# Performance work log

Hardware: AMD Instinct MI355X
Metric: run time of the kernel (lower is better)

Reference implementation:

```python
import jax, jax.numpy as jnp
import numpy as np
from jax import lax

C = 256  # out_channels
K2 = 1   # a_kernel_size // 2


def _alpha_weights():
    # generate_alpha_weights(dilation=1): (2, 3) constant
    s = float(np.sin(-np.pi / 4.0))
    c = float(np.cos(-np.pi / 4.0))
    aw = np.zeros((2, 3), dtype=np.float32)
    aw[0, 0] = c
    aw[1, 0] = -s
    aw[0, -1] = s
    aw[1, -1] = c
    return jnp.asarray(aw)


def setup_inputs() -> dict:
    key = jax.random.key(0)
    k1, k2, k3 = jax.random.split(key, 3)
    x = jax.random.normal(k1, (32, 256, 64, 64), dtype=jnp.float32)
    w = jax.random.normal(k2, (256, 256, 3, 3), dtype=jnp.float32) * 0.05
    alpha = jax.random.normal(k3, (C, K2, 2, 2), dtype=jnp.float32) * 0.5
    return {"x": x, "w": w, "alpha": alpha}


def _arma_forward(x, w, alpha):
    # moving-average: Conv2d 3x3, stride 1, zero padding 1, no bias
    y = lax.conv_general_dilated(
        x, w, window_strides=(1, 1), padding=[(1, 1), (1, 1)],
        dimension_numbers=("NCHW", "OIHW", "NCHW"))
    B, Co, H, W = y.shape

    aw = _alpha_weights()  # (2, 3)
    at = jnp.tanh(alpha)                       # (C, K2, 2, 2)
    A_xy = jnp.einsum('ckab,bj->ckaj', at, aw)  # (C, K2, 2, 3)
    A_xy = A_xy.at[:, :, :, 1].set(1.0)         # middle tap forced to 1
    A_x = A_xy[:, :, 0:1, :]                    # (C, K2, 1, 3)
    A_y = A_xy[:, :, 1:2, :]                    # (C, K2, 1, 3)
    A = jnp.einsum('ckai,ckbj->ckij', A_x, A_y)  # (C, K2, 3, 3) separable 2D filter
    # pad to (C, K2, H, W) then roll so the center tap sits at the origin
    A_pad = jnp.pad(A, ((0, 0), (0, 0), (0, H - 3), (0, W - 3)))
    A_roll = jnp.roll(A_pad, shift=(-1, -1), axis=(-2, -1))

    # circular AR recursion via frequency-domain division, per dilation chunk
    for k in range(K2):
        a = A_roll[:, k]                        # (C, H, W)
        Yf = jnp.fft.fft2(y) / jnp.fft.fft2(a)  # broadcast (B,C,H,W)/(C,H,W)
        y = jnp.real(jnp.fft.ifft2(Yf))
    return y


def reference(x, w, alpha):
    return _arma_forward(x, w, alpha)
```

## Files before the change

### kernel.cpp

```cpp
#include <hip/hip_runtime.h>
#include <cmath>
#include <stdint.h>

#define HH 64
#define WD 64
#define CIN 256
#define COUT 256
#define NB 32

typedef _Float16 half8 __attribute__((ext_vector_type(8)));
typedef _Float16 half4 __attribute__((ext_vector_type(4)));
typedef float floatx4 __attribute__((ext_vector_type(4)));

#define SB() __builtin_amdgcn_sched_barrier(0)

__device__ __forceinline__ void glds16(const void* src, void* dst) {
    __builtin_amdgcn_global_load_lds((const __attribute__((address_space(1))) void*)src,
                                     (__attribute__((address_space(3))) void*)dst, 16, 0, 0);
}

__global__ __launch_bounds__(256) void xprep_kernel(const float* __restrict__ x,
                                                    _Float16* __restrict__ x16) {
    __shared__ _Float16 lt[32 * 72];
    const int tid = threadIdx.x;
    const int bid = blockIdx.x;
    const int h = bid & 63;
    const int chunk = (bid >> 6) & 7;
    const int n = bid >> 9;
    {
        const int ci = tid >> 3;
        const int w8 = (tid & 7) * 8;
        const float* src = x + (((size_t)(n * 256 + chunk * 32 + ci) * 64 + h) * 64 + w8);
        const float4 a = *(const float4*)src;
        const float4 b = *(const float4*)(src + 4);
        half8 hv;
        hv[0] = (_Float16)a.x; hv[1] = (_Float16)a.y; hv[2] = (_Float16)a.z; hv[3] = (_Float16)a.w;
        hv[4] = (_Float16)b.x; hv[5] = (_Float16)b.y; hv[6] = (_Float16)b.z; hv[7] = (_Float16)b.w;
        *(half8*)&lt[ci * 72 + w8] = hv;
    }
    __syncthreads();
    {
        const int w = tid >> 2;
        const int kc = tid & 3;
        half8 hv;
        #pragma unroll
        for (int j = 0; j < 8; ++j) hv[j] = lt[(kc * 8 + j) * 72 + w];
        *(half8*)&x16[(((size_t)(n * 8 + chunk) * 64 + h) * 64 + w) * 32 + kc * 8] = hv;
    }
}

__global__ __launch_bounds__(256) void wprep_kernel(const float* __restrict__ w,
                                                    _Float16* __restrict__ w16,
                                                    float4* __restrict__ zp) {
    const int idx = blockIdx.x * 256 + threadIdx.x;
    const int j = idx & 7;
    const int m = (idx >> 3) & 15;
    const int q = (idx >> 7) & 3;
    const int u = (idx >> 9) & 3;
    const int rest = idx >> 11;
    const int tap = rest % 9;
    const int rr = rest / 9;
    const int cb = rr & 3;
    const int chunk = rr >> 2;
    const int co = cb * 64 + u * 16 + m;
    const int ci = chunk * 32 + q * 8 + j;
    w16[idx] = (_Float16)w[(co * CIN + ci) * 9 + tap];
    if (blockIdx.x == 0) {
        float4 z; z.x = 0.f; z.y = 0.f; z.z = 0.f; z.w = 0.f;
        zp[threadIdx.x] = z;
    }
}

__global__ __launch_bounds__(256) void gprep1_kernel(const float* __restrict__ alpha,
                                                     float* __restrict__ gtab) {
    const int gid = blockIdx.x * 256 + threadIdx.x;
    const int r   = gid & 63;
    const int isv = (gid >> 6) & 1;
    const int c   = gid >> 7;
    const float t0 = tanhf(alpha[c * 4 + isv * 2 + 0]);
    const float t1 = tanhf(alpha[c * 4 + isv * 2 + 1]);
    const float qq = 0.70710678118654752f;
    const float a0 = qq * (t0 + t1);
    const float a2 = qq * (t1 - t0);
    const float w0 = 0.09817477042468103f;
    float ssum = 0.f;
    for (int p = 0; p < 64; ++p) {
        const float th = w0 * (float)p;
        const float re = 1.f + (a0 + a2) * cosf(th);
        const float im = (a0 - a2) * sinf(th);
        const float inv = 1.f / (re * re + im * im);
        const float ph = w0 * (float)((p * r) & 63);
        ssum += (cosf(ph) * re + sinf(ph) * im) * inv;
    }
    gtab[gid] = ssum * (1.0f / 64.0f);
}

__global__ __launch_bounds__(256) void gprep2_kernel(const float* __restrict__ gtab,
                                                     _Float16* __restrict__ gm) {
    const int idx = blockIdx.x * 256 + threadIdx.x;
    const int kc = idx & 7;
    const int row = (idx >> 3) & 63;
    const int which = (idx >> 9) & 1;
    const int c = idx >> 10;
    const float* g = gtab + c * 128 + which * 64;
    half8 hv;
    #pragma unroll
    for (int j = 0; j < 8; ++j)
        hv[j] = (_Float16)g[(row - (kc * 8 + j)) & 63];
    *(half8*)&gm[((size_t)(c * 2 + which) * 64 + row) * 64 + ((kc ^ (row & 7)) * 8)] = hv;
}

__global__ __launch_bounds__(512, 2) void conv_mfma(const _Float16* __restrict__ x16,
                                                    const _Float16* __restrict__ w16,
                                                    const _Float16* __restrict__ zp,
                                                    float* __restrict__ y) {
    extern __shared__ __align__(16) _Float16 xs2[];
    const int tid  = threadIdx.x;
    const int lane = tid & 63;
    const int wv   = tid >> 6;
    const int m    = lane & 15;
    const int q    = lane >> 4;

    const int hw   = blockIdx.x;
    const int xcd  = hw & 7;
    const int ii   = hw >> 3;
    const int pair = xcd * 16 + (ii >> 2);
    const int cb   = ii & 3;
    const int ht   = pair & 3;
    const int n    = pair >> 2;
    const int h0   = ht * 16;

    const int s_kcs = tid & 3;
    const int s_cx  = ((tid >> 2) & 63) + 1;
    const int s_gw  = s_cx - 1;
    const int s_kc  = s_kcs ^ (s_cx & 3);
    const int s_cxb = ((wv & 3) << 4) + 1;
    const int s_sr0 = wv >> 2;

    int aoff[3];
    #pragma unroll
    for (int kx = 0; kx < 3; ++kx)
        aoff[kx] = (m + kx) * 32 + ((q ^ ((m + kx) & 3)) * 8);

    floatx4 acc[2][4][4];
    #pragma unroll
    for (int ro = 0; ro < 2; ++ro)
        #pragma unroll
        for (int cbk = 0; cbk < 4; ++cbk)
            #pragma unroll
            for (int u = 0; u < 4; ++u) acc[ro][cbk][u] = (floatx4)0.f;

    if (tid < 288) {
        const int b   = tid / 144;
        const int r2  = tid - b * 144;
        const int kcs = r2 & 3;
        const int cxe = ((r2 >> 2) & 1) * 65;
        const int row = r2 >> 3;
        *(half8*)&xs2[b * 38016 + (row * 66 + cxe) * 32 + kcs * 8] = (half8)(_Float16)0.f;
    }

    {
        const _Float16* xc0 = x16 + (size_t)(n * 8 + 0) * 131072;
        #pragma unroll
        for (int it = 0; it < 9; ++it) {
            const int sr = 2 * it + s_sr0;
            const int gh = h0 - 1 + sr;
            const _Float16* src = ((unsigned)gh < 64u)
                ? xc0 + ((gh * 64 + s_gw) * 32 + s_kc * 8)
                : zp + (lane << 3);
            _Float16* dst = xs2 + (sr * 66 + s_cxb) * 32;
            glds16(src, dst);
        }
    }
    asm volatile("s_waitcnt vmcnt(0)" ::: "memory");
    __syncthreads();

    for (int c = 0; c < 8; ++c) {
        _Float16* bcur = xs2 + (c & 1) * 38016;
        _Float16* bnxt = xs2 + ((c & 1) ^ 1) * 38016;
        const _Float16* wchunk = w16 + (size_t)(c * 4 + cb) * 18432;
        const _Float16* xcn = x16 + (size_t)(n * 8 + ((c + 1) & 7)) * 131072;
        const bool pf = (c < 7);

        #pragma unroll
        for (int kx = 0; kx < 3; ++kx) {
            half8 bf[3][4];
            #pragma unroll
            for (int ky = 0; ky < 3; ++ky)
                #pragma unroll
                for (int u = 0; u < 4; ++u)
                    bf[ky][u] = *(const half8*)&wchunk[(ky * 3 + kx) * 2048 + u * 512 + lane * 8];

            if (kx == 0 && pf) {
                SB();
                #pragma unroll
                for (int it = 0; it < 5; ++it) {
                    const int sr = 2 * it + s_sr0;
                    const int gh = h0 - 1 + sr;
                    const _Float16* src = ((unsigned)gh < 64u)
                        ? xcn + ((gh * 64 + s_gw) * 32 + s_kc * 8)
                        : zp + (lane << 3);
                    glds16(src, bnxt + (sr * 66 + s_cxb) * 32);
                }
                SB();
            }
            if (kx == 1 && pf) {
                SB();
                #pragma unroll
                for (int it = 5; it < 9; ++it) {
                    const int sr = 2 * it + s_sr0;
                    const int gh = h0 - 1 + sr;
                    const _Float16* src = ((unsigned)gh < 64u)
                        ? xcn + ((gh * 64 + s_gw) * 32 + s_kc * 8)
                        : zp + (lane << 3);
                    glds16(src, bnxt + (sr * 66 + s_cxb) * 32);
                }
                SB();
            }

            #pragma unroll
            for (int cbk = 0; cbk < 4; ++cbk) {
                half8 af[4];
                #pragma unroll
                for (int rr = 0; rr < 4; ++rr)
                    af[rr] = *(const half8*)&bcur[(wv * 2 + rr) * 2112 + cbk * 512 + aoff[kx]];
                #pragma unroll
                for (int ro = 0; ro < 2; ++ro)
                    #pragma unroll
                    for (int ky = 0; ky < 3; ++ky)
                        #pragma unroll
                        for (int u = 0; u < 4; ++u)
                            acc[ro][cbk][u] = __builtin_amdgcn_mfma_f32_16x16x32_f16(
                                bf[ky][u], af[ro + ky], acc[ro][cbk][u], 0, 0, 0);
            }
        }
        asm volatile("s_waitcnt vmcnt(0)" ::: "memory");
        __syncthreads();
    }

    _Float16* y16o = (_Float16*)y;
    #pragma unroll
    for (int u = 0; u < 4; ++u) {
        #pragma unroll
        for (int r = 0; r < 4; ++r) {
            const int co = cb * 64 + u * 16 + q * 4 + r;
            _Float16* yp = y16o + (size_t)(n * COUT + co) * 8192 + 4096;
            #pragma unroll
            for (int ro = 0; ro < 2; ++ro)
                #pragma unroll
                for (int cbk = 0; cbk < 4; ++cbk)
                    yp[(h0 + wv * 2 + ro) * 64 + cbk * 16 + m] = (_Float16)acc[ro][cbk][u][r];
        }
    }
}

__global__ __launch_bounds__(256, 4) void solve_mfma(const _Float16* __restrict__ gm,
                                                     float* __restrict__ y) {
    __shared__ __align__(16) _Float16 Ys[64 * 64];
    __shared__ __align__(16) _Float16 Tt[64 * 64];
    __shared__ __align__(16) _Float16 Gsh[2 * 64 * 64];
    const int tid  = threadIdx.x;
    const int lane = tid & 63;
    const int wv   = tid >> 6;
    const int m    = lane & 15;
    const int q    = lane >> 4;
    const int plane = blockIdx.x;
    const int c = plane & 255;
    float* yp = y + (size_t)plane * 4096;
    const _Float16* ysrc = (const _Float16*)y + (size_t)plane * 8192 + 4096;

    {
        #pragma unroll
        for (int it = 0; it < 2; ++it) {
            const int s   = it * 256 + tid;
            const int r   = s >> 3;
            const int kcs = s & 7;
            const int kc  = kcs ^ (r & 7);
            const _Float16* src = ysrc + r * 64 + kc * 8;
            _Float16* dst = Ys + (it * 256 + wv * 64) * 8;
            glds16(src, dst);
        }
        const _Float16* gsrc = gm + (size_t)c * 8192;
        #pragma unroll
        for (int it = 0; it < 4; ++it) {
            const _Float16* src = gsrc + (size_t)(it * 256 + tid) * 8;
            _Float16* dst = Gsh + (it * 256 + wv * 64) * 8;
            glds16(src, dst);
        }
    }
    asm volatile("s_waitcnt vmcnt(0)" ::: "memory");
    __syncthreads();

    {
        floatx4 acc1[4];
        #pragma unroll
        for (int u = 0; u < 4; ++u) acc1[u] = (floatx4)0.f;
        #pragma unroll
        for (int ks = 0; ks < 2; ++ks) {
            const int swz = ((ks * 4 + q) ^ (m & 7)) * 8;
            const half8 yf = *(const half8*)&Ys[(16 * wv + m) * 64 + swz];
            #pragma unroll
            for (int u = 0; u < 4; ++u) {
                const half8 gvf = *(const half8*)&Gsh[4096 + (u * 16 + m) * 64 + swz];
                acc1[u] = __builtin_amdgcn_mfma_f32_16x16x32_f16(yf, gvf, acc1[u], 0, 0, 0);
            }
        }
        #pragma unroll
        for (int u = 0; u < 4; ++u) {
            half4 hv;
            #pragma unroll
            for (int r = 0; r < 4; ++r) hv[r] = (_Float16)acc1[u][r];
            const int s = u * 16 + m;
            const int kc = 2 * wv + (q >> 1);
            *(half4*)&Tt[s * 64 + ((kc ^ (s & 7)) * 8) + (q & 1) * 4] = hv;
        }
    }
    __syncthreads();

    {
        floatx4 acc2[4];
        #pragma unroll
        for (int u = 0; u < 4; ++u) acc2[u] = (floatx4)0.f;
        #pragma unroll
        for (int ks = 0; ks < 2; ++ks) {
            const int swz = ((ks * 4 + q) ^ (m & 7)) * 8;
            const half8 guf = *(const half8*)&Gsh[(16 * wv + m) * 64 + swz];
            #pragma unroll
            for (int u = 0; u < 4; ++u) {
                const half8 ttf = *(const half8*)&Tt[(u * 16 + m) * 64 + swz];
                acc2[u] = __builtin_amdgcn_mfma_f32_16x16x32_f16(guf, ttf, acc2[u], 0, 0, 0);
            }
        }
        #pragma unroll
        for (int u = 0; u < 4; ++u)
            #pragma unroll
            for (int r = 0; r < 4; ++r)
                yp[(16 * wv + q * 4 + r) * 64 + u * 16 + m] = acc2[u][r];
    }
}

extern "C" void kernel_launch(void* const* d_in, const int* in_sizes, int n_in,
                              void* d_out, int out_size, void* d_ws, size_t ws_size,
                              hipStream_t stream) {
    const float* x     = (const float*)d_in[0];
    const float* w     = (const float*)d_in[1];
    const float* alpha = (const float*)d_in[2];
    float* y = (float*)d_out;

    _Float16* x16 = (_Float16*)d_ws;
    _Float16* w16 = (_Float16*)((char*)d_ws + 67108864);
    _Float16* gm  = (_Float16*)((char*)d_ws + 68288512);
    float*    gtab = (float*)((char*)d_ws + 72482816);
    float4*   zp   = (float4*)((char*)d_ws + 72613888);

    static bool inited = false;
    if (!inited) {
        hipFuncSetAttribute((const void*)conv_mfma,
                            hipFuncAttributeMaxDynamicSharedMemorySize, 152064);
        inited = true;
    }

    xprep_kernel <<<dim3(32 * 8 * 64), 256, 0, stream>>>(x, x16);
    wprep_kernel <<<dim3(2304),        256, 0, stream>>>(w, w16, zp);
    gprep1_kernel<<<dim3(128),         256, 0, stream>>>(alpha, gtab);
    gprep2_kernel<<<dim3(1024),        256, 0, stream>>>(gtab, gm);
    conv_mfma    <<<dim3(512),         512, 152064, stream>>>(x16, w16, (const _Float16*)zp, y);
    solve_mfma   <<<dim3(NB * COUT),   256, 0, stream>>>(gm, y);
}
```

Before: 403.3 us.

## Retile conv into 256-thread half-width blocks, batch solve planes, use hardware trig

The conv kernel changes from 512-thread blocks covering a 16x64 tile to 256-thread blocks covering a 16x32 tile. Each wave now computes 4 output rows with 2 column blocks, with precomputed staging offsets that zero-fill the halo, plus s_setprio around the MFMA bursts. Halving shared memory per block and doubling the grid should let more blocks fit per CU. The solve kernel now runs 2048 blocks that each handle 4 batch planes for one channel: the G matrix is loaded once and reused, and the next Y plane is double-buffered while the current one computes. gprep1 switches to the hardware sin/cos builtins, which take revolutions and trade some accuracy for speed.

```diff
diff --git a/kernel.cpp b/kernel.cpp
--- a/kernel.cpp
+++ b/kernel.cpp
@@ -82,15 +82,15 @@
     const float qq = 0.70710678118654752f;
     const float a0 = qq * (t0 + t1);
     const float a2 = qq * (t1 - t0);
-    const float w0 = 0.09817477042468103f;
+    const float rev = 0.015625f;
     float ssum = 0.f;
     for (int p = 0; p < 64; ++p) {
-        const float th = w0 * (float)p;
-        const float re = 1.f + (a0 + a2) * cosf(th);
-        const float im = (a0 - a2) * sinf(th);
+        const float pr = (float)p * rev;
+        const float re = 1.f + (a0 + a2) * __builtin_amdgcn_cosf(pr);
+        const float im = (a0 - a2) * __builtin_amdgcn_sinf(pr);
         const float inv = 1.f / (re * re + im * im);
-        const float ph = w0 * (float)((p * r) & 63);
-        ssum += (cosf(ph) * re + sinf(ph) * im) * inv;
+        const float ph = (float)((p * r) & 63) * rev;
+        ssum += (__builtin_amdgcn_cosf(ph) * re + __builtin_amdgcn_sinf(ph) * im) * inv;
     }
     gtab[gid] = ssum * (1.0f / 64.0f);
 }
@@ -110,7 +110,7 @@
     *(half8*)&gm[((size_t)(c * 2 + which) * 64 + row) * 64 + ((kc ^ (row & 7)) * 8)] = hv;
 }
 
-__global__ __launch_bounds__(512, 2) void conv_mfma(const _Float16* __restrict__ x16,
+__global__ __launch_bounds__(256, 2) void conv_mfma(const _Float16* __restrict__ x16,
                                                     const _Float16* __restrict__ w16,
                                                     const _Float16* __restrict__ zp,
                                                     float* __restrict__ y) {
@@ -121,65 +121,63 @@
     const int m    = lane & 15;
     const int q    = lane >> 4;
 
-    const int hw   = blockIdx.x;
-    const int xcd  = hw & 7;
-    const int ii   = hw >> 3;
-    const int pair = xcd * 16 + (ii >> 2);
-    const int cb   = ii & 3;
+    const int bid  = blockIdx.x;
+    const int xcd  = bid & 7;
+    const int idx  = bid >> 3;
+    const int sub  = idx & 7;
+    const int cb   = sub >> 1;
+    const int wt   = sub & 1;
+    const int pair = xcd * 16 + (idx >> 3);
     const int ht   = pair & 3;
     const int n    = pair >> 2;
     const int h0   = ht * 16;
-
-    const int s_kcs = tid & 3;
-    const int s_cx  = ((tid >> 2) & 63) + 1;
-    const int s_gw  = s_cx - 1;
-    const int s_kc  = s_kcs ^ (s_cx & 3);
-    const int s_cxb = ((wv & 3) << 4) + 1;
-    const int s_sr0 = wv >> 2;
+    const int w0   = wt * 32;
+
+    int soff[10];
+    #pragma unroll
+    for (int it = 0; it < 10; ++it) {
+        const int slot = it * 256 + tid;
+        const int row  = (slot * 7711) >> 20;
+        const int rem  = slot - row * 136;
+        const int col  = rem >> 2;
+        const int oct  = (rem & 3) ^ (col & 3);
+        const int gh   = h0 - 1 + row;
+        const int gw   = w0 - 1 + col;
+        soff[it] = ((unsigned)gh < 64u && (unsigned)gw < 64u)
+                 ? ((gh * 64 + gw) * 32 + oct * 8) : -1;
+    }
 
     int aoff[3];
     #pragma unroll
     for (int kx = 0; kx < 3; ++kx)
         aoff[kx] = (m + kx) * 32 + ((q ^ ((m + kx) & 3)) * 8);
 
-    floatx4 acc[2][4][4];
-    #pragma unroll
-    for (int ro = 0; ro < 2; ++ro)
-        #pragma unroll
-        for (int cbk = 0; cbk < 4; ++cbk)
+    floatx4 acc[4][2][4];
+    #pragma unroll
+    for (int ro = 0; ro < 4; ++ro)
+        #pragma unroll
+        for (int cbk = 0; cbk < 2; ++cbk)
             #pragma unroll
             for (int u = 0; u < 4; ++u) acc[ro][cbk][u] = (floatx4)0.f;
 
-    if (tid < 288) {
-        const int b   = tid / 144;
-        const int r2  = tid - b * 144;
-        const int kcs = r2 & 3;
-        const int cxe = ((r2 >> 2) & 1) * 65;
-        const int row = r2 >> 3;
-        *(half8*)&xs2[b * 38016 + (row * 66 + cxe) * 32 + kcs * 8] = (half8)(_Float16)0.f;
-    }
-
-    {
-        const _Float16* xc0 = x16 + (size_t)(n * 8 + 0) * 131072;
-        #pragma unroll
-        for (int it = 0; it < 9; ++it) {
-            const int sr = 2 * it + s_sr0;
-            const int gh = h0 - 1 + sr;
-            const _Float16* src = ((unsigned)gh < 64u)
-                ? xc0 + ((gh * 64 + s_gw) * 32 + s_kc * 8)
-                : zp + (lane << 3);
-            _Float16* dst = xs2 + (sr * 66 + s_cxb) * 32;
-            glds16(src, dst);
+    {
+        const _Float16* xc0 = x16 + (size_t)n * 1048576;
+        #pragma unroll
+        for (int it = 0; it < 10; ++it) {
+            if (it * 256 + tid < 2448) {
+                const _Float16* src = (soff[it] >= 0) ? xc0 + soff[it] : zp + (lane << 3);
+                glds16(src, xs2 + (size_t)(it * 256 + wv * 64) * 8);
+            }
         }
     }
     asm volatile("s_waitcnt vmcnt(0)" ::: "memory");
     __syncthreads();
 
     for (int c = 0; c < 8; ++c) {
-        _Float16* bcur = xs2 + (c & 1) * 38016;
-        _Float16* bnxt = xs2 + ((c & 1) ^ 1) * 38016;
+        _Float16* bcur = xs2 + (c & 1) * 19584;
+        _Float16* bnxt = xs2 + ((c & 1) ^ 1) * 19584;
         const _Float16* wchunk = w16 + (size_t)(c * 4 + cb) * 18432;
-        const _Float16* xcn = x16 + (size_t)(n * 8 + ((c + 1) & 7)) * 131072;
+        const _Float16* xcn = x16 + (size_t)(n * 8 + c + 1) * 131072;
         const bool pf = (c < 7);
 
         #pragma unroll
@@ -195,43 +193,39 @@
                 SB();
                 #pragma unroll
                 for (int it = 0; it < 5; ++it) {
-                    const int sr = 2 * it + s_sr0;
-                    const int gh = h0 - 1 + sr;
-                    const _Float16* src = ((unsigned)gh < 64u)
-                        ? xcn + ((gh * 64 + s_gw) * 32 + s_kc * 8)
-                        : zp + (lane << 3);
-                    glds16(src, bnxt + (sr * 66 + s_cxb) * 32);
+                    const _Float16* src = (soff[it] >= 0) ? xcn + soff[it] : zp + (lane << 3);
+                    glds16(src, bnxt + (size_t)(it * 256 + wv * 64) * 8);
                 }
                 SB();
             }
             if (kx == 1 && pf) {
                 SB();
                 #pragma unroll
-                for (int it = 5; it < 9; ++it) {
-                    const int sr = 2 * it + s_sr0;
-                    const int gh = h0 - 1 + sr;
-                    const _Float16* src = ((unsigned)gh < 64u)
-                        ? xcn + ((gh * 64 + s_gw) * 32 + s_kc * 8)
-                        : zp + (lane << 3);
-                    glds16(src, bnxt + (sr * 66 + s_cxb) * 32);
+                for (int it = 5; it < 10; ++it) {
+                    if (it * 256 + tid < 2448) {
+                        const _Float16* src = (soff[it] >= 0) ? xcn + soff[it] : zp + (lane << 3);
+                        glds16(src, bnxt + (size_t)(it * 256 + wv * 64) * 8);
+                    }
                 }
                 SB();
             }
 
             #pragma unroll
-            for (int cbk = 0; cbk < 4; ++cbk) {
-                half8 af[4];
-                #pragma unroll
-                for (int rr = 0; rr < 4; ++rr)
-                    af[rr] = *(const half8*)&bcur[(wv * 2 + rr) * 2112 + cbk * 512 + aoff[kx]];
-                #pragma unroll
-                for (int ro = 0; ro < 2; ++ro)
+            for (int cbk = 0; cbk < 2; ++cbk) {
+                half8 af[6];
+                #pragma unroll
+                for (int rr = 0; rr < 6; ++rr)
+                    af[rr] = *(const half8*)&bcur[(wv * 4 + rr) * 1088 + cbk * 512 + aoff[kx]];
+                __builtin_amdgcn_s_setprio(1);
+                #pragma unroll
+                for (int ro = 0; ro < 4; ++ro)
                     #pragma unroll
                     for (int ky = 0; ky < 3; ++ky)
                         #pragma unroll
                         for (int u = 0; u < 4; ++u)
                             acc[ro][cbk][u] = __builtin_amdgcn_mfma_f32_16x16x32_f16(
                                 bf[ky][u], af[ro + ky], acc[ro][cbk][u], 0, 0, 0);
+                __builtin_amdgcn_s_setprio(0);
             }
         }
         asm volatile("s_waitcnt vmcnt(0)" ::: "memory");
@@ -246,17 +240,17 @@
             const int co = cb * 64 + u * 16 + q * 4 + r;
             _Float16* yp = y16o + (size_t)(n * COUT + co) * 8192 + 4096;
             #pragma unroll
-            for (int ro = 0; ro < 2; ++ro)
-                #pragma unroll
-                for (int cbk = 0; cbk < 4; ++cbk)
-                    yp[(h0 + wv * 2 + ro) * 64 + cbk * 16 + m] = (_Float16)acc[ro][cbk][u][r];
+            for (int ro = 0; ro < 4; ++ro)
+                #pragma unroll
+                for (int cbk = 0; cbk < 2; ++cbk)
+                    yp[(h0 + wv * 4 + ro) * 64 + w0 + cbk * 16 + m] = (_Float16)acc[ro][cbk][u][r];
         }
     }
 }
 
 __global__ __launch_bounds__(256, 4) void solve_mfma(const _Float16* __restrict__ gm,
                                                      float* __restrict__ y) {
-    __shared__ __align__(16) _Float16 Ys[64 * 64];
+    __shared__ __align__(16) _Float16 Ysd[2][64 * 64];
     __shared__ __align__(16) _Float16 Tt[64 * 64];
     __shared__ __align__(16) _Float16 Gsh[2 * 64 * 64];
     const int tid  = threadIdx.x;
@@ -264,78 +258,94 @@
     const int wv   = tid >> 6;
     const int m    = lane & 15;
     const int q    = lane >> 4;
-    const int plane = blockIdx.x;
-    const int c = plane & 255;
-    float* yp = y + (size_t)plane * 4096;
-    const _Float16* ysrc = (const _Float16*)y + (size_t)plane * 8192 + 4096;
-
-    {
+    const int bid  = blockIdx.x;
+    const int nq   = bid & 7;
+    const int c    = bid >> 3;
+
+    {
+        const _Float16* gsrc = gm + (size_t)c * 8192;
+        #pragma unroll
+        for (int it = 0; it < 4; ++it)
+            glds16(gsrc + (size_t)(it * 256 + tid) * 8, Gsh + (size_t)(it * 256 + wv * 64) * 8);
+    }
+    {
+        const _Float16* ysrc = (const _Float16*)y + ((size_t)(nq * 4 + 0) * 256 + c) * 8192 + 4096;
         #pragma unroll
         for (int it = 0; it < 2; ++it) {
-            const int s   = it * 256 + tid;
-            const int r   = s >> 3;
-            const int kcs = s & 7;
-            const int kc  = kcs ^ (r & 7);
-            const _Float16* src = ysrc + r * 64 + kc * 8;
-            _Float16* dst = Ys + (it * 256 + wv * 64) * 8;
-            glds16(src, dst);
-        }
-        const _Float16* gsrc = gm + (size_t)c * 8192;
-        #pragma unroll
-        for (int it = 0; it < 4; ++it) {
-            const _Float16* src = gsrc + (size_t)(it * 256 + tid) * 8;
-            _Float16* dst = Gsh + (it * 256 + wv * 64) * 8;
-            glds16(src, dst);
+            const int s  = it * 256 + tid;
+            const int r  = s >> 3;
+            const int kc = (s & 7) ^ (r & 7);
+            glds16(ysrc + r * 64 + kc * 8, Ysd[0] + (size_t)(it * 256 + wv * 64) * 8);
         }
     }
     asm volatile("s_waitcnt vmcnt(0)" ::: "memory");
     __syncthreads();
 
-    {
-        floatx4 acc1[4];
-        #pragma unroll
-        for (int u = 0; u < 4; ++u) acc1[u] = (floatx4)0.f;
-        #pragma unroll
-        for (int ks = 0; ks < 2; ++ks) {
-            const int swz = ((ks * 4 + q) ^ (m & 7)) * 8;
-            const half8 yf = *(const half8*)&Ys[(16 * wv + m) * 64 + swz];
+    #pragma unroll
+    for (int i = 0; i < 4; ++i) {
+        const _Float16* Ys = Ysd[i & 1];
+        if (i < 3) {
+            const _Float16* ysrc = (const _Float16*)y + ((size_t)(nq * 4 + i + 1) * 256 + c) * 8192 + 4096;
+            #pragma unroll
+            for (int it = 0; it < 2; ++it) {
+                const int s  = it * 256 + tid;
+                const int r  = s >> 3;
+                const int kc = (s & 7) ^ (r & 7);
+                glds16(ysrc + r * 64 + kc * 8, Ysd[(i & 1) ^ 1] + (size_t)(it * 256 + wv * 64) * 8);
+            }
+        }
+
+        {
+            floatx4 acc1[4];
+            #pragma unroll
+            for (int u = 0; u < 4; ++u) acc1[u] = (floatx4)0.f;
+            #pragma unroll
+            for (int ks = 0; ks < 2; ++ks) {
+                const int swz = ((ks * 4 + q) ^ (m & 7)) * 8;
+                const half8 yf = *(const half8*)&Ys[(16 * wv + m) * 64 + swz];
+                #pragma unroll
+                for (int u = 0; u < 4; ++u) {
+                    const half8 gvf = *(const half8*)&Gsh[4096 + (u * 16 + m) * 64 + swz];
+                    acc1[u] = __builtin_amdgcn_mfma_f32_16x16x32_f16(yf, gvf, acc1[u], 0, 0, 0);
+                }
+            }
             #pragma unroll
             for (int u = 0; u < 4; ++u) {
-                const half8 gvf = *(const half8*)&Gsh[4096 + (u * 16 + m) * 64 + swz];
-                acc1[u] = __builtin_amdgcn_mfma_f32_16x16x32_f16(yf, gvf, acc1[u], 0, 0, 0);
-            }
-        }
-        #pragma unroll
-        for (int u = 0; u < 4; ++u) {
-            half4 hv;
-            #pragma unroll
-            for (int r = 0; r < 4; ++r) hv[r] = (_Float16)acc1[u][r];
-            const int s = u * 16 + m;
-            const int kc = 2 * wv + (q >> 1);
-            *(half4*)&Tt[s * 64 + ((kc ^ (s & 7)) * 8) + (q & 1) * 4] = hv;
-        }
-    }
-    __syncthreads();
-
-    {
-        floatx4 acc2[4];
-        #pragma unroll
-        for (int u = 0; u < 4; ++u) acc2[u] = (floatx4)0.f;
-        #pragma unroll
-        for (int ks = 0; ks < 2; ++ks) {
-            const int swz = ((ks * 4 + q) ^ (m & 7)) * 8;
-            const half8 guf = *(const half8*)&Gsh[(16 * wv + m) * 64 + swz];
-            #pragma unroll
-            for (int u = 0; u < 4; ++u) {
-                const half8 ttf = *(const half8*)&Tt[(u * 16 + m) * 64 + swz];
-                acc2[u] = __builtin_amdgcn_mfma_f32_16x16x32_f16(guf, ttf, acc2[u], 0, 0, 0);
-            }
-        }
-        #pragma unroll
-        for (int u = 0; u < 4; ++u)
-            #pragma unroll
-            for (int r = 0; r < 4; ++r)
-                yp[(16 * wv + q * 4 + r) * 64 + u * 16 + m] = acc2[u][r];
+                half4 hv;
+                #pragma unroll
+                for (int r = 0; r < 4; ++r) hv[r] = (_Float16)acc1[u][r];
+                const int s = u * 16 + m;
+                const int kc = 2 * wv + (q >> 1);
+                *(half4*)&Tt[s * 64 + ((kc ^ (s & 7)) * 8) + (q & 1) * 4] = hv;
+            }
+        }
+        __syncthreads();
+
+        {
+            float* yp = y + ((size_t)(nq * 4 + i) * 256 + c) * 4096;
+            floatx4 acc2[4];
+            #pragma unroll
+            for (int u = 0; u < 4; ++u) acc2[u] = (floatx4)0.f;
+            #pragma unroll
+            for (int ks = 0; ks < 2; ++ks) {
+                const int swz = ((ks * 4 + q) ^ (m & 7)) * 8;
+                const half8 guf = *(const half8*)&Gsh[(16 * wv + m) * 64 + swz];
+                #pragma unroll
+                for (int u = 0; u < 4; ++u) {
+                    const half8 ttf = *(const half8*)&Tt[(u * 16 + m) * 64 + swz];
+                    acc2[u] = __builtin_amdgcn_mfma_f32_16x16x32_f16(guf, ttf, acc2[u], 0, 0, 0);
+                }
+            }
+            #pragma unroll
+            for (int u = 0; u < 4; ++u)
+                #pragma unroll
+                for (int r = 0; r < 4; ++r)
+                    yp[(16 * wv + q * 4 + r) * 64 + u * 16 + m] = acc2[u][r];
+        }
+        if (i < 3) {
+            asm volatile("s_waitcnt vmcnt(0)" ::: "memory");
+            __syncthreads();
+        }
     }
 }
 
@@ -356,7 +366,7 @@
     static bool inited = false;
     if (!inited) {
         hipFuncSetAttribute((const void*)conv_mfma,
-                            hipFuncAttributeMaxDynamicSharedMemorySize, 152064);
+                            hipFuncAttributeMaxDynamicSharedMemorySize, 78336);
         inited = true;
     }
 
@@ -364,6 +374,6 @@
     wprep_kernel <<<dim3(2304),        256, 0, stream>>>(w, w16, zp);
     gprep1_kernel<<<dim3(128),         256, 0, stream>>>(alpha, gtab);
     gprep2_kernel<<<dim3(1024),        256, 0, stream>>>(gtab, gm);
-    conv_mfma    <<<dim3(512),         512, 152064, stream>>>(x16, w16, (const _Float16*)zp, y);
-    solve_mfma   <<<dim3(NB * COUT),   256, 0, stream>>>(gm, y);
-}
+    conv_mfma    <<<dim3(1024),        256, 78336, stream>>>(x16, w16, (const _Float16*)zp, y);
+    solve_mfma   <<<dim3(2048),        256, 0, stream>>>(gm, y);
+}
```

After: 390.4 us. 3.2% less time.
